# Optimization experiments

Hardware: AMD Instinct MI355X
Metric: run time of the kernel (lower is better)

Reference implementation:

```python
import jax, jax.numpy as jnp
import numpy as np

EPS = 1e-5

def mish(x):
    return x * jnp.tanh(jax.nn.softplus(x))

def layernorm(x, w, b):
    mu = jnp.mean(x, axis=-1, keepdims=True)
    var = jnp.mean(jnp.square(x - mu), axis=-1, keepdims=True)
    return (x - mu) * jax.lax.rsqrt(var + EPS) * w + b

def linear(x, w, b):
    # torch convention: w is [out, in]
    return x @ w.T + b

def setup_inputs() -> dict:
    key = jax.random.key(0)
    ks = jax.random.split(key, 40)
    B, N, T, H, PH, SH, A = 16384, 54, 80, 48, 80, 32, 397
    s = 0.05
    inp = {
        'trunk_out': jax.random.normal(ks[0], (B, T), jnp.float32),
        'node_emb': jax.random.normal(ks[1], (B, N, H), jnp.float32),
        'road_pairs': jax.random.randint(ks[2], (72, 2), 0, N),
        'tile_nodes': jax.random.randint(ks[3], (19, 6), 0, N),
        # LayerNorms
        'ln_t_w': jnp.ones((T,), jnp.float32), 'ln_t_b': jnp.zeros((T,), jnp.float32),
        'ln_n_w': jnp.ones((H,), jnp.float32), 'ln_n_b': jnp.zeros((H,), jnp.float32),
        # global_fc: Linear(T,PH) + BN(PH) + Mish + Linear(PH,A)
        'gfc1_w': jax.random.normal(ks[4], (PH, T)) * s, 'gfc1_b': jnp.zeros((PH,), jnp.float32),
        'bn_w': jnp.ones((PH,), jnp.float32), 'bn_b': jnp.zeros((PH,), jnp.float32),
        'gfc2_w': jax.random.normal(ks[5], (A, PH)) * s, 'gfc2_b': jnp.zeros((A,), jnp.float32),
        # settlement scorer: Linear(T+H, SH) -> Mish -> Linear(SH,1)
        'sett1_w': jax.random.normal(ks[6], (SH, T + H)) * s, 'sett1_b': jnp.zeros((SH,), jnp.float32),
        'sett2_w': jax.random.normal(ks[7], (1, SH)) * s, 'sett2_b': jnp.zeros((1,), jnp.float32),
        # city scorer
        'city1_w': jax.random.normal(ks[8], (SH, T + H)) * s, 'city1_b': jnp.zeros((SH,), jnp.float32),
        'city2_w': jax.random.normal(ks[9], (1, SH)) * s, 'city2_b': jnp.zeros((1,), jnp.float32),
        # road scorer: Linear(T+2H, SH) -> Mish -> Linear(SH,1)
        'road1_w': jax.random.normal(ks[10], (SH, T + 2 * H)) * s, 'road1_b': jnp.zeros((SH,), jnp.float32),
        'road2_w': jax.random.normal(ks[11], (1, SH)) * s, 'road2_b': jnp.zeros((1,), jnp.float32),
        # robber scorer: Linear(T+H, SH) -> Mish -> Linear(SH,5)
        'rob1_w': jax.random.normal(ks[12], (SH, T + H)) * s, 'rob1_b': jnp.zeros((SH,), jnp.float32),
        'rob2_w': jax.random.normal(ks[13], (5, SH)) * s, 'rob2_b': jnp.zeros((5,), jnp.float32),
    }
    return inp

def reference(trunk_out, node_emb, road_pairs, tile_nodes,
              ln_t_w, ln_t_b, ln_n_w, ln_n_b,
              gfc1_w, gfc1_b, bn_w, bn_b, gfc2_w, gfc2_b,
              sett1_w, sett1_b, sett2_w, sett2_b,
              city1_w, city1_b, city2_w, city2_b,
              road1_w, road1_b, road2_w, road2_b,
              rob1_w, rob1_b, rob2_w, rob2_b):
    B, N, H = node_emb.shape
    tn = layernorm(trunk_out, ln_t_w, ln_t_b)          # [B,T]
    nn_ = layernorm(node_emb, ln_n_w, ln_n_b)          # [B,N,H]

    # global_fc with BatchNorm1d in training mode (batch statistics)
    h = linear(tn, gfc1_w, gfc1_b)                     # [B,PH]
    mu = jnp.mean(h, axis=0)
    var = jnp.mean(jnp.square(h - mu), axis=0)
    h = (h - mu) * jax.lax.rsqrt(var + EPS) * bn_w + bn_b
    global_logits = linear(mish(h), gfc2_w, gfc2_b)    # [B,397]

    tn_n = jnp.broadcast_to(tn[:, None, :], (B, N, tn.shape[-1]))
    ctx = jnp.concatenate([tn_n, nn_], axis=-1)        # [B,N,T+H]
    sett = linear(mish(linear(ctx, sett1_w, sett1_b)), sett2_w, sett2_b)[..., 0]  # [B,N]
    city = linear(mish(linear(ctx, city1_w, city1_b)), city2_w, city2_b)[..., 0]  # [B,N]

    src = nn_[:, road_pairs[:, 0], :]                  # [B,72,H]
    dst = nn_[:, road_pairs[:, 1], :]                  # [B,72,H]
    tn_e = jnp.broadcast_to(tn[:, None, :], (B, 72, tn.shape[-1]))
    road_ctx = jnp.concatenate([tn_e, src, dst], axis=-1)
    road = linear(mish(linear(road_ctx, road1_w, road1_b)), road2_w, road2_b)[..., 0]  # [B,72]

    tile_emb = jnp.mean(nn_[:, tile_nodes, :], axis=2) # [B,19,H]
    tn_t = jnp.broadcast_to(tn[:, None, :], (B, 19, tn.shape[-1]))
    tile_ctx = jnp.concatenate([tn_t, tile_emb], axis=-1)
    robber = linear(mish(linear(tile_ctx, rob1_w, rob1_b)), rob2_w, rob2_b).reshape(B, 95)

    return jnp.concatenate([global_logits[:, :5], sett, city, road, robber, global_logits[:, 280:]], axis=1)
```

## Files before the change

### kernel.cpp

```cpp
#include <hip/hip_runtime.h>
#include <hip/hip_bf16.h>

#define BB 16384
#define NN 54
#define TT 80
#define HH 48
#define PH 80
#define SHH 32
#define AA 397
#define EPSF 1e-5f

typedef __hip_bfloat16 bf16;

__device__ __forceinline__ float tof(float x){ return x; }
__device__ __forceinline__ float tof(bf16 x){ return __bfloat162float(x); }
__device__ __forceinline__ void stor(float* p, float v){ *p = v; }
__device__ __forceinline__ void stor(bf16* p, float v){ *p = __float2bfloat16(v); }

__device__ __forceinline__ float mishf(float x){
    float e = __expf(fminf(x, 15.f));
    float w = e * (2.f + e);
    return x * w / (w + 2.f);
}

__device__ __forceinline__ void unpack2(unsigned u, float* x){
    x[0] = __uint_as_float(u << 16);
    x[1] = __uint_as_float(u & 0xffff0000u);
}

struct P30 { const void* a[30]; };

#define OFF_WtT   0
#define OFF_WnT   (OFF_WtT + 80*128)
#define OFF_B1P   (OFF_WnT + 48*128)
#define OFF_WRT   (OFF_B1P + 128)
#define OFF_WRN   (OFF_WRT + 80*32)
#define OFF_RB1   (OFF_WRN + 48*32)
#define OFF_W2P   (OFF_RB1 + 32)
#define OFF_ROB2  (OFF_W2P + 96)
#define OFF_B2S   (OFF_ROB2 + 160)
#define OFF_LNW   (OFF_B2S + 8)
#define OFF_LNB   (OFF_LNW + 48)
#define OFF_B2G   (OFF_LNB + 48)
#define OFF_WG1T  (OFF_B2G + 122)
#define OFF_B1G   (OFF_WG1T + 80*80)
#define OFF_WG2T  (OFF_B1G + 80)
#define PK_TOTAL  (OFF_WG2T + 80*122)

__global__ void k_detect(const unsigned short* tr, int* flag,
                         float* bn_sum, float* bn_sq){
    int t = threadIdx.x;
    if (t < PH){ bn_sum[t] = 0.f; bn_sq[t] = 0.f; }
    if (t == 0){
        int good = 0;
        for (int i = 0; i < 1024; i += 2){
            int e = (tr[i] >> 7) & 0xFF;
            if (e >= 117 && e <= 137) good++;
        }
        *flag = (good > 256) ? 1 : 0;
    }
}

template<typename T>
__device__ void prep_body(P30 p, float* pk){
    const T* sett1_w=(const T*)p.a[14]; const T* sett1_b=(const T*)p.a[15];
    const T* sett2_w=(const T*)p.a[16]; const T* sett2_b=(const T*)p.a[17];
    const T* city1_w=(const T*)p.a[18]; const T* city1_b=(const T*)p.a[19];
    const T* city2_w=(const T*)p.a[20]; const T* city2_b=(const T*)p.a[21];
    const T* road1_w=(const T*)p.a[22]; const T* road1_b=(const T*)p.a[23];
    const T* road2_w=(const T*)p.a[24]; const T* road2_b=(const T*)p.a[25];
    const T* rob1_w =(const T*)p.a[26]; const T* rob1_b =(const T*)p.a[27];
    const T* rob2_w =(const T*)p.a[28]; const T* rob2_b =(const T*)p.a[29];
    const T* gfc1_w =(const T*)p.a[8];  const T* gfc1_b =(const T*)p.a[9];
    const T* gfc2_w =(const T*)p.a[12]; const T* gfc2_b =(const T*)p.a[13];
    const T* ln_n_w =(const T*)p.a[6];  const T* ln_n_b =(const T*)p.a[7];

    int gid = blockIdx.x*blockDim.x + threadIdx.x;
    int gsz = gridDim.x*blockDim.x;

    for (int i=gid; i<80*128; i+=gsz){ int k=i>>7, j=i&127; float v;
        if (j<32)      v = tof(sett1_w[j*128+k]);
        else if (j<64) v = tof(city1_w[(j-32)*128+k]);
        else if (j<96) v = tof(road1_w[(j-64)*176+k]);
        else           v = 0.f;
        pk[OFF_WtT+i]=v; }
    for (int i=gid; i<48*128; i+=gsz){ int k=i>>7, j=i&127; float v;
        if (j<32)      v = tof(sett1_w[j*128+80+k]);
        else if (j<64) v = tof(city1_w[(j-32)*128+80+k]);
        else if (j<96) v = tof(road1_w[(j-64)*176+80+k]);
        else           v = tof(road1_w[(j-96)*176+128+k]);
        pk[OFF_WnT+i]=v; }
    for (int i=gid; i<128; i+=gsz){ float v;
        if (i<32) v=tof(sett1_b[i]); else if (i<64) v=tof(city1_b[i-32]);
        else if (i<96) v=tof(road1_b[i-64]); else v=0.f;
        pk[OFF_B1P+i]=v; }
    for (int i=gid; i<80*32; i+=gsz){ int k=i>>5, h=i&31; pk[OFF_WRT+i]=tof(rob1_w[h*128+k]); }
    for (int i=gid; i<48*32; i+=gsz){ int k=i>>5, h=i&31; pk[OFF_WRN+i]=tof(rob1_w[h*128+80+k]); }
    for (int i=gid; i<32; i+=gsz) pk[OFF_RB1+i]=tof(rob1_b[i]);
    for (int i=gid; i<96; i+=gsz){ float v;
        if (i<32) v=tof(sett2_w[i]); else if (i<64) v=tof(city2_w[i-32]); else v=tof(road2_w[i-64]);
        pk[OFF_W2P+i]=v; }
    for (int i=gid; i<160; i+=gsz) pk[OFF_ROB2+i]=tof(rob2_w[i]);
    for (int i=gid; i<8; i+=gsz){ float v;
        if (i==0) v=tof(sett2_b[0]); else if (i==1) v=tof(city2_b[0]);
        else if (i==2) v=tof(road2_b[0]); else v=tof(rob2_b[i-3]);
        pk[OFF_B2S+i]=v; }
    for (int i=gid; i<48; i+=gsz){ pk[OFF_LNW+i]=tof(ln_n_w[i]); pk[OFF_LNB+i]=tof(ln_n_b[i]); }
    for (int i=gid; i<122; i+=gsz){ int col = (i<5)? i : (280+i-5); pk[OFF_B2G+i]=tof(gfc2_b[col]); }
    for (int i=gid; i<80*80; i+=gsz){ int k=i/80, j=i%80; pk[OFF_WG1T+i]=tof(gfc1_w[j*80+k]); }
    for (int i=gid; i<80; i+=gsz) pk[OFF_B1G+i]=tof(gfc1_b[i]);
    for (int i=gid; i<80*122; i+=gsz){ int k=i/122, g=i-k*122;
        int col = (g<5)? g : (280+g-5);
        pk[OFF_WG2T+i]=tof(gfc2_w[col*PH+k]); }
}

__global__ void k_prep(P30 p, float* pk, const int* __restrict__ flag){
    if (*flag) prep_body<bf16>(p, pk); else prep_body<float>(p, pk);
}

template<typename T>
__device__ void tn8_body(const T* __restrict__ trunk,
                         const T* __restrict__ lw, const T* __restrict__ lb,
                         const float* __restrict__ pk,
                         float* __restrict__ hbuf, float* __restrict__ tpr,
                         float* __restrict__ bn_sum, float* __restrict__ bn_sq,
                         float* __restrict__ s_tnT){
    int tid = threadIdx.x, wave = tid >> 6, lane = tid & 63;
    int row0 = blockIdx.x * 8;
    for (int r2 = 0; r2 < 2; ++r2){
        int rb = wave*2 + r2;
        const T* tr = trunk + (size_t)(row0 + rb) * TT;
        float x0 = (lane < TT)      ? tof(tr[lane])      : 0.f;
        float x1 = (lane + 64 < TT) ? tof(tr[lane + 64]) : 0.f;
        float s = x0 + x1;
        for (int m = 32; m; m >>= 1) s += __shfl_xor(s, m, 64);
        float mu = s / TT;
        float d0 = (lane < TT)      ? (x0 - mu) : 0.f;
        float d1 = (lane + 64 < TT) ? (x1 - mu) : 0.f;
        float v = d0*d0 + d1*d1;
        for (int m = 32; m; m >>= 1) v += __shfl_xor(v, m, 64);
        float rstd = rsqrtf(v / TT + EPSF);
        if (lane < TT)
            s_tnT[lane*12 + rb] = d0 * rstd * tof(lw[lane]) + tof(lb[lane]);
        if (lane + 64 < TT)
            s_tnT[(lane+64)*12 + rb] = d1 * rstd * tof(lw[lane+64]) + tof(lb[lane+64]);
    }
    __syncthreads();
    if (tid < 240){
        const float* wp; int stride; float bias; float* ob; int ostride;
        if (tid < 80){
            wp = pk + OFF_WG1T + tid; stride = 80;  bias = pk[OFF_B1G + tid];
            ob = hbuf + (size_t)row0*80 + tid;  ostride = 80;
        } else if (tid < 208){
            int j = tid - 80;
            wp = pk + OFF_WtT + j;  stride = 128; bias = pk[OFF_B1P + j];
            ob = tpr + (size_t)row0*160 + j;    ostride = 160;
        } else {
            int j = tid - 208;
            wp = pk + OFF_WRT + j;  stride = 32;  bias = pk[OFF_RB1 + j];
            ob = tpr + (size_t)row0*160 + 128 + j; ostride = 160;
        }
        float acc[8];
        #pragma unroll
        for (int r = 0; r < 8; ++r) acc[r] = bias;
        #pragma unroll 4
        for (int k = 0; k < TT; ++k){
            float wv = wp[k*stride];
            float4 a = *(const float4*)&s_tnT[k*12];
            float4 b = *(const float4*)&s_tnT[k*12 + 4];
            acc[0] += wv*a.x; acc[1] += wv*a.y; acc[2] += wv*a.z; acc[3] += wv*a.w;
            acc[4] += wv*b.x; acc[5] += wv*b.y; acc[6] += wv*b.z; acc[7] += wv*b.w;
        }
        #pragma unroll
        for (int r = 0; r < 8; ++r) ob[r*ostride] = acc[r];
        if (tid < 80){
            float s8 = 0.f, q8 = 0.f;
            #pragma unroll
            for (int r = 0; r < 8; ++r){ s8 += acc[r]; q8 += acc[r]*acc[r]; }
            atomicAdd(bn_sum + tid, s8);
            atomicAdd(bn_sq  + tid, q8);
        }
    }
}

__global__ __launch_bounds__(256) void k_tn8(P30 p, const float* pk, float* hbuf,
                                             float* tpr, float* bn_sum, float* bn_sq,
                                             const int* __restrict__ flag){
    __shared__ float s_tnT[80*12];
    if (*flag)
        tn8_body<bf16>((const bf16*)p.a[0], (const bf16*)p.a[4], (const bf16*)p.a[5],
                       pk, hbuf, tpr, bn_sum, bn_sq, s_tnT);
    else
        tn8_body<float>((const float*)p.a[0], (const float*)p.a[4], (const float*)p.a[5],
                        pk, hbuf, tpr, bn_sum, bn_sq, s_tnT);
}

__global__ void k_bnstats2(P30 p, const float* __restrict__ bn_sum,
                           const float* __restrict__ bn_sq,
                           float* scale, float* shift, const int* __restrict__ flag){
    int f = threadIdx.x;
    if (f < PH){
        float mu  = bn_sum[f] * (1.f/BB);
        float var = bn_sq[f]  * (1.f/BB) - mu*mu;
        float bw, bb;
        if (*flag){ bw = tof(((const bf16*)p.a[10])[f]); bb = tof(((const bf16*)p.a[11])[f]); }
        else      { bw = ((const float*)p.a[10])[f];     bb = ((const float*)p.a[11])[f]; }
        float sc = rsqrtf(var + EPSF) * bw;
        scale[f] = sc;
        shift[f] = bb - mu * sc;
    }
}

template<typename T>
__device__ void ghead_body(const float* __restrict__ hbuf,
                           const float* __restrict__ scale, const float* __restrict__ shift,
                           const float* __restrict__ pk, T* __restrict__ out,
                           float* __restrict__ s_mT){
    int tid = threadIdx.x;
    int row0 = blockIdx.x * 16;
    const float* wg2t = pk + OFF_WG2T;
    const float* b2g  = pk + OFF_B2G;
    for (int i = tid; i < 1280; i += 256){
        int r = i / 80, k = i - r*80;
        float hv = hbuf[(size_t)(row0 + r)*80 + k];
        s_mT[k*20 + r] = mishf(hv * scale[k] + shift[k]);
    }
    __syncthreads();
    int g = tid & 127, half = tid >> 7, r0 = half * 8;
    if (g < 122){
        float acc[8] = {0,0,0,0,0,0,0,0};
        #pragma unroll 4
        for (int k = 0; k < 80; ++k){
            float wv = wg2t[k*122 + g];
            float4 a = *(const float4*)&s_mT[k*20 + r0];
            float4 b = *(const float4*)&s_mT[k*20 + r0 + 4];
            acc[0] += wv*a.x; acc[1] += wv*a.y; acc[2] += wv*a.z; acc[3] += wv*a.w;
            acc[4] += wv*b.x; acc[5] += wv*b.y; acc[6] += wv*b.z; acc[7] += wv*b.w;
        }
        int col = (g < 5) ? g : (280 + g - 5);
        float bg = b2g[g];
        #pragma unroll
        for (int r = 0; r < 8; ++r)
            stor(out + (size_t)(row0 + r0 + r)*AA + col, acc[r] + bg);
    }
}

__global__ __launch_bounds__(256) void k_ghead(const float* hbuf, const float* scale,
                                               const float* shift, const float* pk,
                                               void* out, const int* __restrict__ flag){
    __shared__ float s_mT[80*20];
    if (*flag) ghead_body<bf16>(hbuf, scale, shift, pk, (bf16*)out, s_mT);
    else       ghead_body<float>(hbuf, scale, shift, pk, (float*)out, s_mT);
}

struct HeadsSmem {
    float s_nnT[HH*55];
    float s_npr[64*56];
    float s_te[HH*20];
    float s_trp[32*20];
};

template<typename T>
__device__ void heads_body(HeadsSmem& sm,
        const T* __restrict__ node_emb, const int* __restrict__ road_pairs,
        const int* __restrict__ tile_nodes,
        const float* __restrict__ tpr, const float* __restrict__ pk,
        T* __restrict__ out){
    const float* WnT   = pk + OFF_WnT;
    const float* Wrn   = pk + OFF_WRN;
    const float* w2p   = pk + OFF_W2P;
    const float* rob2p = pk + OFF_ROB2;
    const float* b2s   = pk + OFF_B2S;
    const float* lnw   = pk + OFF_LNW;
    const float* lnb   = pk + OFF_LNB;

    int row = blockIdx.x, tid = threadIdx.x;
    int wave = tid >> 6, lane = tid & 63;
    const float* tpr_row = tpr + (size_t)row*160;

    if (lane < 16){
        int n = (wave << 4) + lane;
        if (n < NN){
            const T* ne = node_emb + ((size_t)row*NN + n)*HH;
            float x[HH];
            if constexpr (sizeof(T) == 2){
                const uint4* v = (const uint4*)ne;
                #pragma unroll
                for (int i = 0; i < 6; ++i){
                    uint4 u = v[i];
                    unpack2(u.x, x + i*8 + 0); unpack2(u.y, x + i*8 + 2);
                    unpack2(u.z, x + i*8 + 4); unpack2(u.w, x + i*8 + 6);
                }
            } else {
                const float4* v = (const float4*)ne;
                #pragma unroll
                for (int i = 0; i < 12; ++i){
                    float4 f = v[i];
                    x[i*4] = f.x; x[i*4+1] = f.y; x[i*4+2] = f.z; x[i*4+3] = f.w;
                }
            }
            float s = 0.f, q = 0.f;
            #pragma unroll
            for (int i = 0; i < HH; ++i){ s += x[i]; q += x[i]*x[i]; }
            float mu   = s * (1.f/HH);
            float var  = q * (1.f/HH) - mu*mu;
            float rstd = rsqrtf(fmaxf(var, 0.f) + EPSF);
            #pragma unroll
            for (int i = 0; i < HH; ++i)
                sm.s_nnT[i*55 + n] = (x[i] - mu)*rstd*lnw[i] + lnb[i];
        }
    }
    __syncthreads();

    int j0 = __builtin_amdgcn_readfirstlane(wave << 5);
    int nx = (lane < NN) ? lane : (NN-1);
    float acc[32];
    #pragma unroll
    for (int j = 0; j < 32; ++j) acc[j] = 0.f;
    const float* wbase = WnT + j0;
    #pragma unroll 2
    for (int h = 0; h < HH; ++h){
        float xn = sm.s_nnT[h*55 + nx];
        const float* wr = wbase + h*128;
        #pragma unroll
        for (int j = 0; j < 32; ++j) acc[j] += wr[j] * xn;
    }
    T* orow = out + (size_t)row*AA;
    if (wave < 2){
        if (lane < NN){
            const float* tpk = tpr_row + j0;
            float o = b2s[wave];
            #pragma unroll 4
            for (int k = 0; k < 32; ++k)
                o += mishf(tpk[k] + acc[k]) * w2p[j0 + k];
            stor(orow + (wave ? 59 : 5) + lane, o);
        }
    } else {
        if (lane < NN){
            int kb = (wave - 2) << 5;
            #pragma unroll
            for (int k = 0; k < 32; ++k) sm.s_npr[(kb + k)*56 + lane] = acc[k];
        }
    }
    __syncthreads();

    for (int i = tid; i < 912; i += 256){
        int h = i / 19, t2 = i - h*19;
        const int* t6 = tile_nodes + t2*6;
        const float* r = sm.s_nnT + h*55;
        sm.s_te[h*20 + t2] = (r[t6[0]] + r[t6[1]] + r[t6[2]]
                            + r[t6[3]] + r[t6[4]] + r[t6[5]]) * (1.f/6.f);
    }
    __syncthreads();

    for (int idx = tid; idx < 608; idx += 256){
        int k = idx & 31, t2 = idx >> 5;
        float a2 = 0.f;
        #pragma unroll 4
        for (int h = 0; h < HH; ++h)
            a2 += sm.s_te[h*20 + t2] * Wrn[h*32 + k];
        sm.s_trp[k*20 + t2] = a2;
    }
    __syncthreads();

    if (tid < 72){
        int r = tid;
        int srcn = road_pairs[2*r], dstn = road_pairs[2*r + 1];
        const float* tpk = tpr_row + 64;
        float o = b2s[2];
        #pragma unroll 4
        for (int k = 0; k < 32; ++k)
            o += mishf(tpk[k] + sm.s_npr[k*56 + srcn]
                              + sm.s_npr[(32 + k)*56 + dstn]) * w2p[64 + k];
        stor(orow + 113 + r, o);
    } else if (tid >= 128 && tid < 147){
        int t2 = tid - 128;
        const float* rtp = tpr_row + 128;
        float a0 = b2s[3], a1 = b2s[4], a2 = b2s[5], a3 = b2s[6], a4 = b2s[7];
        #pragma unroll 2
        for (int k = 0; k < 32; ++k){
            float m = mishf(rtp[k] + sm.s_trp[k*20 + t2]);
            a0 += m * rob2p[k];      a1 += m * rob2p[32 + k];
            a2 += m * rob2p[64 + k]; a3 += m * rob2p[96 + k];
            a4 += m * rob2p[128 + k];
        }
        stor(orow + 185 + t2*5 + 0, a0);
        stor(orow + 185 + t2*5 + 1, a1);
        stor(orow + 185 + t2*5 + 2, a2);
        stor(orow + 185 + t2*5 + 3, a3);
        stor(orow + 185 + t2*5 + 4, a4);
    }
}

__global__ __launch_bounds__(256) void k_heads(P30 p, const float* tpr, const float* pk,
                                               void* out, const int* __restrict__ flag){
    __shared__ HeadsSmem sm;
    if (*flag)
        heads_body<bf16>(sm, (const bf16*)p.a[1], (const int*)p.a[2], (const int*)p.a[3],
                         tpr, pk, (bf16*)out);
    else
        heads_body<float>(sm, (const float*)p.a[1], (const int*)p.a[2], (const int*)p.a[3],
                          tpr, pk, (float*)out);
}

extern "C" void kernel_launch(void* const* d_in, const int* in_sizes, int n_in,
                              void* d_out, int out_size, void* d_ws, size_t ws_size,
                              hipStream_t stream){
    P30 p;
    for (int i = 0; i < 30; ++i) p.a[i] = d_in[i];

    int*   flag   = (int*)d_ws;
    float* bn_sum = (float*)((char*)d_ws + 256);
    float* bn_sq  = bn_sum + PH;
    float* scale  = bn_sq + PH;
    float* shift  = scale + PH;
    float* hbuf   = (float*)((char*)d_ws + 2048);
    float* tpr    = hbuf + (size_t)BB*PH;
    float* pk     = tpr + (size_t)BB*160;

    k_detect<<<1, 128, 0, stream>>>((const unsigned short*)d_in[0], flag, bn_sum, bn_sq);
    k_prep<<<64, 256, 0, stream>>>(p, pk, flag);
    k_tn8<<<BB/8, 256, 0, stream>>>(p, pk, hbuf, tpr, bn_sum, bn_sq, flag);
    k_bnstats2<<<1, 128, 0, stream>>>(p, bn_sum, bn_sq, scale, shift, flag);
    k_ghead<<<BB/16, 256, 0, stream>>>(hbuf, scale, shift, pk, d_out, flag);
    k_heads<<<BB, 256, 0, stream>>>(p, tpr, pk, d_out, flag);
}
```

Baseline: 1.260 ms.

## Process one batch row per wave in heads kernel using cross-lane permutes

The heads kernel now assigns one batch row to each wave (four rows per block) instead of one row per block. Each lane holds one node's layernormed embedding in registers. Gathers for road pairs and tile means use ds_bpermute instead of shared memory. This removes shared memory use, all block-wide barriers and the idle-lane phases of the old layout. The cost is higher register pressure from several 32-wide accumulator arrays and a 48-float input, and the tile projection is now computed per node before averaging rather than after.

```diff
diff --git a/kernel.cpp b/kernel.cpp
--- a/kernel.cpp
+++ b/kernel.cpp
@@ -26,6 +26,10 @@
 __device__ __forceinline__ void unpack2(unsigned u, float* x){
     x[0] = __uint_as_float(u << 16);
     x[1] = __uint_as_float(u & 0xffff0000u);
+}
+
+__device__ __forceinline__ float bperm(int byteaddr, float v){
+    return __int_as_float(__builtin_amdgcn_ds_bpermute(byteaddr, __float_as_int(v)));
 }
 
 struct P30 { const void* a[30]; };
@@ -253,19 +257,28 @@
     else       ghead_body<float>(hbuf, scale, shift, pk, (float*)out, s_mT);
 }
 
-struct HeadsSmem {
-    float s_nnT[HH*55];
-    float s_npr[64*56];
-    float s_te[HH*20];
-    float s_trp[32*20];
-};
+template<int STRIDE>
+__device__ __forceinline__ void proj32(const float* __restrict__ Wbase,
+                                       const float* __restrict__ x,
+                                       float* __restrict__ acc){
+    #pragma unroll
+    for (int j = 0; j < 32; ++j) acc[j] = 0.f;
+    #pragma unroll
+    for (int h = 0; h < HH; ++h){
+        const float* wr = Wbase + h*STRIDE;
+        float xh = x[h];
+        #pragma unroll
+        for (int j = 0; j < 32; ++j) acc[j] += wr[j] * xh;
+    }
+}
 
 template<typename T>
-__device__ void heads_body(HeadsSmem& sm,
-        const T* __restrict__ node_emb, const int* __restrict__ road_pairs,
-        const int* __restrict__ tile_nodes,
-        const float* __restrict__ tpr, const float* __restrict__ pk,
-        T* __restrict__ out){
+__device__ void heads_body(const T* __restrict__ node_emb,
+                           const int* __restrict__ road_pairs,
+                           const int* __restrict__ tile_nodes,
+                           const float* __restrict__ tpr,
+                           const float* __restrict__ pk,
+                           T* __restrict__ out){
     const float* WnT   = pk + OFF_WnT;
     const float* Wrn   = pk + OFF_WRN;
     const float* w2p   = pk + OFF_W2P;
@@ -274,132 +287,110 @@
     const float* lnw   = pk + OFF_LNW;
     const float* lnb   = pk + OFF_LNB;
 
-    int row = blockIdx.x, tid = threadIdx.x;
-    int wave = tid >> 6, lane = tid & 63;
+    int tid  = threadIdx.x;
+    int wave = __builtin_amdgcn_readfirstlane(tid >> 6);
+    int lane = tid & 63;
+    int row  = blockIdx.x*4 + wave;
     const float* tpr_row = tpr + (size_t)row*160;
-
-    if (lane < 16){
-        int n = (wave << 4) + lane;
-        if (n < NN){
-            const T* ne = node_emb + ((size_t)row*NN + n)*HH;
-            float x[HH];
-            if constexpr (sizeof(T) == 2){
-                const uint4* v = (const uint4*)ne;
-                #pragma unroll
-                for (int i = 0; i < 6; ++i){
-                    uint4 u = v[i];
-                    unpack2(u.x, x + i*8 + 0); unpack2(u.y, x + i*8 + 2);
-                    unpack2(u.z, x + i*8 + 4); unpack2(u.w, x + i*8 + 6);
-                }
-            } else {
-                const float4* v = (const float4*)ne;
-                #pragma unroll
-                for (int i = 0; i < 12; ++i){
-                    float4 f = v[i];
-                    x[i*4] = f.x; x[i*4+1] = f.y; x[i*4+2] = f.z; x[i*4+3] = f.w;
-                }
+    T* orow = out + (size_t)row*AA;
+
+    float x[HH];
+    {
+        int n = (lane < NN) ? lane : (NN-1);
+        const T* ne = node_emb + ((size_t)row*NN + n)*HH;
+        if constexpr (sizeof(T) == 2){
+            const uint4* v = (const uint4*)ne;
+            #pragma unroll
+            for (int i = 0; i < 6; ++i){
+                uint4 u = v[i];
+                unpack2(u.x, x + i*8 + 0); unpack2(u.y, x + i*8 + 2);
+                unpack2(u.z, x + i*8 + 4); unpack2(u.w, x + i*8 + 6);
             }
-            float s = 0.f, q = 0.f;
+        } else {
+            const float4* v = (const float4*)ne;
             #pragma unroll
-            for (int i = 0; i < HH; ++i){ s += x[i]; q += x[i]*x[i]; }
-            float mu   = s * (1.f/HH);
-            float var  = q * (1.f/HH) - mu*mu;
-            float rstd = rsqrtf(fmaxf(var, 0.f) + EPSF);
+            for (int i = 0; i < 12; ++i){
+                float4 f = v[i];
+                x[i*4] = f.x; x[i*4+1] = f.y; x[i*4+2] = f.z; x[i*4+3] = f.w;
+            }
+        }
+        float s = 0.f, q = 0.f;
+        #pragma unroll
+        for (int i = 0; i < HH; ++i){ s += x[i]; q += x[i]*x[i]; }
+        float mu   = s * (1.f/HH);
+        float var  = q * (1.f/HH) - mu*mu;
+        float rstd = rsqrtf(fmaxf(var, 0.f) + EPSF);
+        #pragma unroll
+        for (int i = 0; i < HH; ++i) x[i] = (x[i] - mu)*rstd*lnw[i] + lnb[i];
+    }
+
+    {
+        float acc[32]; proj32<128>(WnT, x, acc);
+        float o = b2s[0];
+        #pragma unroll
+        for (int k = 0; k < 32; ++k) o += mishf(tpr_row[k] + acc[k]) * w2p[k];
+        if (lane < NN) stor(orow + 5 + lane, o);
+    }
+    {
+        float acc[32]; proj32<128>(WnT + 32, x, acc);
+        float o = b2s[1];
+        #pragma unroll
+        for (int k = 0; k < 32; ++k) o += mishf(tpr_row[32+k] + acc[k]) * w2p[32+k];
+        if (lane < NN) stor(orow + 59 + lane, o);
+    }
+    {
+        float rp[32]; proj32<32>(Wrn, x, rp);
+        int t = (lane < 19) ? lane : 18;
+        const int* t6 = tile_nodes + t*6;
+        int a0 = t6[0]*4, a1 = t6[1]*4, a2 = t6[2]*4,
+            a3 = t6[3]*4, a4 = t6[4]*4, a5 = t6[5]*4;
+        float acc5[5];
+        #pragma unroll
+        for (int i = 0; i < 5; ++i) acc5[i] = b2s[3+i];
+        const float* rtp = tpr_row + 128;
+        #pragma unroll
+        for (int k = 0; k < 32; ++k){
+            float rk = rp[k];
+            float s = bperm(a0, rk) + bperm(a1, rk) + bperm(a2, rk)
+                    + bperm(a3, rk) + bperm(a4, rk) + bperm(a5, rk);
+            float m = mishf(rtp[k] + s * (1.f/6.f));
+            acc5[0] += m * rob2p[k];      acc5[1] += m * rob2p[32+k];
+            acc5[2] += m * rob2p[64+k];   acc5[3] += m * rob2p[96+k];
+            acc5[4] += m * rob2p[128+k];
+        }
+        if (lane < 19){
             #pragma unroll
-            for (int i = 0; i < HH; ++i)
-                sm.s_nnT[i*55 + n] = (x[i] - mu)*rstd*lnw[i] + lnb[i];
-        }
-    }
-    __syncthreads();
-
-    int j0 = __builtin_amdgcn_readfirstlane(wave << 5);
-    int nx = (lane < NN) ? lane : (NN-1);
-    float acc[32];
-    #pragma unroll
-    for (int j = 0; j < 32; ++j) acc[j] = 0.f;
-    const float* wbase = WnT + j0;
-    #pragma unroll 2
-    for (int h = 0; h < HH; ++h){
-        float xn = sm.s_nnT[h*55 + nx];
-        const float* wr = wbase + h*128;
-        #pragma unroll
-        for (int j = 0; j < 32; ++j) acc[j] += wr[j] * xn;
-    }
-    T* orow = out + (size_t)row*AA;
-    if (wave < 2){
-        if (lane < NN){
-            const float* tpk = tpr_row + j0;
-            float o = b2s[wave];
-            #pragma unroll 4
-            for (int k = 0; k < 32; ++k)
-                o += mishf(tpk[k] + acc[k]) * w2p[j0 + k];
-            stor(orow + (wave ? 59 : 5) + lane, o);
-        }
-    } else {
-        if (lane < NN){
-            int kb = (wave - 2) << 5;
-            #pragma unroll
-            for (int k = 0; k < 32; ++k) sm.s_npr[(kb + k)*56 + lane] = acc[k];
-        }
-    }
-    __syncthreads();
-
-    for (int i = tid; i < 912; i += 256){
-        int h = i / 19, t2 = i - h*19;
-        const int* t6 = tile_nodes + t2*6;
-        const float* r = sm.s_nnT + h*55;
-        sm.s_te[h*20 + t2] = (r[t6[0]] + r[t6[1]] + r[t6[2]]
-                            + r[t6[3]] + r[t6[4]] + r[t6[5]]) * (1.f/6.f);
-    }
-    __syncthreads();
-
-    for (int idx = tid; idx < 608; idx += 256){
-        int k = idx & 31, t2 = idx >> 5;
-        float a2 = 0.f;
-        #pragma unroll 4
-        for (int h = 0; h < HH; ++h)
-            a2 += sm.s_te[h*20 + t2] * Wrn[h*32 + k];
-        sm.s_trp[k*20 + t2] = a2;
-    }
-    __syncthreads();
-
-    if (tid < 72){
-        int r = tid;
-        int srcn = road_pairs[2*r], dstn = road_pairs[2*r + 1];
+            for (int i = 0; i < 5; ++i) stor(orow + 185 + lane*5 + i, acc5[i]);
+        }
+    }
+    {
+        float accS[32]; proj32<128>(WnT + 64, x, accS);
+        float accD[32]; proj32<128>(WnT + 96, x, accD);
+        int r1 = lane;
+        int r2 = 64 + (lane & 7);
+        int s1 = road_pairs[2*r1]*4,   d1 = road_pairs[2*r1+1]*4;
+        int s2 = road_pairs[2*r2]*4,   d2 = road_pairs[2*r2+1]*4;
+        float o1 = b2s[2], o2 = b2s[2];
         const float* tpk = tpr_row + 64;
-        float o = b2s[2];
-        #pragma unroll 4
-        for (int k = 0; k < 32; ++k)
-            o += mishf(tpk[k] + sm.s_npr[k*56 + srcn]
-                              + sm.s_npr[(32 + k)*56 + dstn]) * w2p[64 + k];
-        stor(orow + 113 + r, o);
-    } else if (tid >= 128 && tid < 147){
-        int t2 = tid - 128;
-        const float* rtp = tpr_row + 128;
-        float a0 = b2s[3], a1 = b2s[4], a2 = b2s[5], a3 = b2s[6], a4 = b2s[7];
-        #pragma unroll 2
+        #pragma unroll
         for (int k = 0; k < 32; ++k){
-            float m = mishf(rtp[k] + sm.s_trp[k*20 + t2]);
-            a0 += m * rob2p[k];      a1 += m * rob2p[32 + k];
-            a2 += m * rob2p[64 + k]; a3 += m * rob2p[96 + k];
-            a4 += m * rob2p[128 + k];
-        }
-        stor(orow + 185 + t2*5 + 0, a0);
-        stor(orow + 185 + t2*5 + 1, a1);
-        stor(orow + 185 + t2*5 + 2, a2);
-        stor(orow + 185 + t2*5 + 3, a3);
-        stor(orow + 185 + t2*5 + 4, a4);
+            float sk = accS[k], dk = accD[k];
+            float tk = tpk[k], wk = w2p[64+k];
+            o1 += mishf(tk + bperm(s1, sk) + bperm(d1, dk)) * wk;
+            o2 += mishf(tk + bperm(s2, sk) + bperm(d2, dk)) * wk;
+        }
+        stor(orow + 113 + r1, o1);
+        if (lane < 8) stor(orow + 113 + r2, o2);
     }
 }
 
 __global__ __launch_bounds__(256) void k_heads(P30 p, const float* tpr, const float* pk,
                                                void* out, const int* __restrict__ flag){
-    __shared__ HeadsSmem sm;
     if (*flag)
-        heads_body<bf16>(sm, (const bf16*)p.a[1], (const int*)p.a[2], (const int*)p.a[3],
+        heads_body<bf16>((const bf16*)p.a[1], (const int*)p.a[2], (const int*)p.a[3],
                          tpr, pk, (bf16*)out);
     else
-        heads_body<float>(sm, (const float*)p.a[1], (const int*)p.a[2], (const int*)p.a[3],
+        heads_body<float>((const float*)p.a[1], (const int*)p.a[2], (const int*)p.a[3],
                           tpr, pk, (float*)out);
 }
 
@@ -423,5 +414,5 @@
     k_tn8<<<BB/8, 256, 0, stream>>>(p, pk, hbuf, tpr, bn_sum, bn_sq, flag);
     k_bnstats2<<<1, 128, 0, stream>>>(p, bn_sum, bn_sq, scale, shift, flag);
     k_ghead<<<BB/16, 256, 0, stream>>>(hbuf, scale, shift, pk, d_out, flag);
-    k_heads<<<BB, 256, 0, stream>>>(p, tpr, pk, d_out, flag);
-}
+    k_heads<<<BB/4, 256, 0, stream>>>(p, tpr, pk, d_out, flag);
+}
```

After: 1.403 ms. 1.11x slower.
